# Performance work log

Hardware: AMD Instinct MI355X
Metric: run time of the kernel (lower is better)

## Reference

```python
import jax, jax.numpy as jnp
import numpy as np

B, L, D, H = 4, 2048, 512, 8
DH = D // H

def cdist(x):
    # torch.cdist(x, x) with p=2: (b,l,l) euclidean distances over feature dim
    sq = jnp.sum(x * x, axis=-1)  # (b,l)
    d2 = sq[:, :, None] + sq[:, None, :] - 2.0 * jnp.einsum('bld,bmd->blm', x, x)
    return jnp.sqrt(jnp.maximum(d2, 0.0))

def distance_residual_bias(cd, mask2d):
    # raw_max=True branch
    Dm = cd * mask2d
    row_max = jnp.max(Dm, axis=-1, keepdims=True)  # (b,l,1)
    Dm = row_max - Dm
    eye = jnp.eye(Dm.shape[-1], dtype=Dm.dtype)
    Dm = Dm * (1.0 - eye)  # zero diagonal
    return Dm * mask2d

def layernorm(x, g, b, eps=1e-5):
    mu = jnp.mean(x, axis=-1, keepdims=True)
    var = jnp.mean((x - mu) ** 2, axis=-1, keepdims=True)
    return (x - mu) * jax.lax.rsqrt(var + eps) * g + b

def setup_inputs() -> dict:
    key = jax.random.key(0)
    ks = jax.random.split(key, 16)
    s = lambda k, shape: jax.random.normal(k, shape, dtype=jnp.float32) * 0.02
    inp = {
        'x': jax.random.normal(ks[0], (B, L, D), dtype=jnp.float32),
        'node_mask': jnp.ones((B, L), dtype=jnp.float32),
        'wq': s(ks[1], (D, D)), 'bq': jnp.zeros((D,), jnp.float32),
        'wk': s(ks[2], (D, D)), 'bk': jnp.zeros((D,), jnp.float32),
        'wv': s(ks[3], (D, D)), 'bv': jnp.zeros((D,), jnp.float32),
        'wo': s(ks[4], (D, D)), 'bo': jnp.zeros((D,), jnp.float32),
        'ln1_g': jnp.ones((D,), jnp.float32), 'ln1_b': jnp.zeros((D,), jnp.float32),
        'w1': s(ks[5], (D, 4 * D)), 'b1': jnp.zeros((4 * D,), jnp.float32),
        'w2': s(ks[6], (4 * D, D)), 'b2': jnp.zeros((D,), jnp.float32),
        'ln2_g': jnp.ones((D,), jnp.float32), 'ln2_b': jnp.zeros((D,), jnp.float32),
    }
    return inp

def reference(x, node_mask, wq, bq, wk, bk, wv, bv, wo, bo,
              ln1_g, ln1_b, w1, b1, w2, b2, ln2_g, ln2_b):
    b, l, d = x.shape
    mask2d = node_mask[:, :, None] * node_mask[:, None, :]  # (b,l,l)
    bias = distance_residual_bias(cdist(x), mask2d)          # (b,l,l)

    q = (x @ wq + bq).reshape(b, l, H, DH).transpose(0, 2, 1, 3)
    k = (x @ wk + bk).reshape(b, l, H, DH).transpose(0, 2, 1, 3)
    v = (x @ wv + bv).reshape(b, l, H, DH).transpose(0, 2, 1, 3)
    scores = jnp.einsum('bhqd,bhkd->bhqk', q, k) / jnp.sqrt(jnp.float32(DH))
    scores = scores + bias[:, None, :, :]  # broadcast distance bias over heads
    attn = jax.nn.softmax(scores, axis=-1)
    y = jnp.einsum('bhqk,bhkd->bhqd', attn, v).transpose(0, 2, 1, 3).reshape(b, l, d)
    y = y @ wo + bo

    X = layernorm(x + y, ln1_g, ln1_b)            # AddNorm 1 (dropout=eval/no-op)
    ffn = jax.nn.relu(X @ w1 + b1) @ w2 + b2      # PositionWiseFFN
    X = layernorm(X + ffn, ln2_g, ln2_b)          # AddNorm 2
    return X
```

## Files before the change

### kernel.cpp

```cpp
#include <hip/hip_runtime.h>
#include <stdint.h>

#define GAS __attribute__((address_space(1)))
#define LAS __attribute__((address_space(3)))

typedef __attribute__((ext_vector_type(8))) __bf16 bf16x8;
typedef __attribute__((ext_vector_type(4))) float f32x4;

static constexpr int Bb = 4, Ll = 2048, Dd = 512, Hh = 8, DHd = 64;
static constexpr float LOG2E = 1.4426950408889634f;

__device__ __forceinline__ unsigned short f2bf(float f){
  unsigned u = __float_as_uint(f);
  u += 0x7fffu + ((u >> 16) & 1u);
  return (unsigned short)(u >> 16);
}
__device__ __forceinline__ void gload16(const void* g, void* l){
  __builtin_amdgcn_global_load_lds((const GAS void*)g, (LAS void*)l, 16, 0, 0);
}
__device__ __forceinline__ f32x4 mfma16(bf16x8 a, bf16x8 b, f32x4 c){
  return __builtin_amdgcn_mfma_f32_16x16x32_bf16(a, b, c, 0, 0, 0);
}
__device__ __forceinline__ float exp2_hw(float x){
  float r; asm("v_exp_f32 %0, %1" : "=v"(r) : "v"(x)); return r;
}

__global__ __launch_bounds__(256) void sumsq_cast(const float* __restrict__ x,
                                                  unsigned short* __restrict__ xbf,
                                                  float* __restrict__ sq){
  int row = blockIdx.x, tid = threadIdx.x;
  float2 v = ((const float2*)(x + (size_t)row * Dd))[tid];
  ((unsigned*)(xbf + (size_t)row * Dd))[tid] =
      (unsigned)f2bf(v.x) | ((unsigned)f2bf(v.y) << 16);
  float s2 = v.x * v.x + v.y * v.y;
  #pragma unroll
  for (int t = 1; t < 64; t <<= 1) s2 += __shfl_xor(s2, t, 64);
  __shared__ float red[4];
  if ((tid & 63) == 0) red[tid >> 6] = s2;
  __syncthreads();
  if (tid == 0) sq[row] = red[0] + red[1] + red[2] + red[3];
}

__global__ void transpose_all(
    const float* __restrict__ wq, const float* __restrict__ wk,
    const float* __restrict__ wv, const float* __restrict__ wo,
    const float* __restrict__ w1, const float* __restrict__ w2,
    unsigned short* __restrict__ wqkvT, unsigned short* __restrict__ woT,
    unsigned short* __restrict__ w1T, unsigned short* __restrict__ w2T)
{
  __shared__ float t[32][33];
  int bid = blockIdx.x;
  const float* in; unsigned short* out; int R, C, bx, by;
  if (bid < 1024){
    int s = bid >> 8, tt = bid & 255;
    in  = s == 0 ? wq : s == 1 ? wk : s == 2 ? wv : wo;
    out = s == 3 ? woT : wqkvT + s * 512 * 512;
    R = 512; C = 512; bx = tt & 15; by = tt >> 4;
  } else if (bid < 2048){
    int tt = bid - 1024; in = w1; out = w1T; R = 512; C = 2048; bx = tt & 63; by = tt >> 6;
  } else {
    int tt = bid - 2048; in = w2; out = w2T; R = 2048; C = 512; bx = tt & 15; by = tt >> 4;
  }
  int tx = threadIdx.x, ty = threadIdx.y;
  int c0 = bx * 32, r0 = by * 32;
  #pragma unroll
  for (int j = 0; j < 32; j += 8) t[ty + j][tx] = in[(size_t)(r0 + ty + j) * C + c0 + tx];
  __syncthreads();
  #pragma unroll
  for (int j = 0; j < 32; j += 8) out[(size_t)(c0 + ty + j) * R + r0 + tx] = f2bf(t[tx][ty + j]);
}

__global__ __launch_bounds__(256) void v_transpose(const unsigned short* __restrict__ qkv,
                                                   unsigned short* __restrict__ vT){
  int b = blockIdx.z, h = blockIdx.y, l0 = blockIdx.x * 64;
  int tid = threadIdx.x;
  __shared__ unsigned short t[64 * 64];
  #pragma unroll
  for (int it = 0; it < 2; ++it){
    int row = tid >> 2;
    int c = (tid & 3) + it * 4;
    uint4 d = *(const uint4*)(qkv + (size_t)(b * Ll + l0 + row) * 1536 + 1024 + h * DHd + c * 8);
    *(uint4*)((char*)t + row * 128 + ((c ^ (row & 7)) << 4)) = d;
  }
  __syncthreads();
  #pragma unroll
  for (int it = 0; it < 2; ++it){
    int dh = tid >> 2;
    int c2 = (tid & 3) + it * 4;
    unsigned pk[4];
    #pragma unroll
    for (int p = 0; p < 4; ++p){
      unsigned short e0, e1;
      {
        int ll = c2 * 8 + p * 2;
        e0 = *(const unsigned short*)((const char*)t + ll * 128 +
              ((((dh >> 3) ^ (ll & 7))) << 4) + ((dh & 7) << 1));
        ll = c2 * 8 + p * 2 + 1;
        e1 = *(const unsigned short*)((const char*)t + ll * 128 +
              ((((dh >> 3) ^ (ll & 7))) << 4) + ((dh & 7) << 1));
      }
      pk[p] = (unsigned)e0 | ((unsigned)e1 << 16);
    }
    uint4 o; o.x = pk[0]; o.y = pk[1]; o.z = pk[2]; o.w = pk[3];
    *(uint4*)(vT + ((size_t)(b * Hh + h) * DHd + dh) * Ll + l0 + c2 * 8) = o;
  }
}

template<int MODE>
__global__ __launch_bounds__(256) void gemm_bt(
    const unsigned short* __restrict__ A,
    const unsigned short* __restrict__ Bt,
    int M, int N, int K,
    const float* __restrict__ bias,
    const float* __restrict__ extra,
    float* __restrict__ outf,
    unsigned short* __restrict__ outb,
    const float* __restrict__ sq,
    float* __restrict__ rmax,
    const float* __restrict__ mask,
    const float* __restrict__ bias_k,
    const float* __restrict__ bias_v)
{
  int m0, n0, bxx = 0, byy = 0;
  if (MODE == 0){
    int z = blockIdx.z;
    A    += (size_t)z * Ll * Dd;
    Bt    = A;
    outb += (size_t)z * Ll * Ll;
    sq += z * Ll; rmax += z * Ll; mask += z * Ll;
    int tt = blockIdx.x, byv = 0;
    while (tt >= 16 - byv){ tt -= 16 - byv; byv++; }
    byy = byv; bxx = byv + tt;
    m0 = byy * 128; n0 = bxx * 128;
  } else {
    m0 = blockIdx.y * 128; n0 = blockIdx.x * 128;
  }
  if (MODE == 6){
    int z = blockIdx.z;
    A    += (size_t)z * (K >> 1);
    Bt   += (size_t)z * (K >> 1);
    outf += (size_t)z * (size_t)M * N;
  }
  const int KL = (MODE == 6) ? (K >> 1) : K;
  const int tid = threadIdx.x, w = tid >> 6, l = tid & 63;
  const int wm = w >> 1, wn = w & 1;
  __shared__ unsigned short lA[2][128 * 64];
  __shared__ unsigned short lB[2][128 * 64];
  f32x4 acc[4][4];
  const f32x4 z4 = {0.f, 0.f, 0.f, 0.f};
  #pragma unroll
  for (int i = 0; i < 4; i++){
    #pragma unroll
    for (int j = 0; j < 4; j++) acc[i][j] = z4;
  }
  const int srow = w * 8 + (l >> 3);
  const int sc = l & 7;

  #pragma unroll
  for (int j = 0; j < 4; j++){
    int row = j * 32 + srow;
    gload16(A + (size_t)(m0 + row) * K + ((sc ^ (row & 7)) << 3),
            &lA[0][0] + j * 2048 + w * 512);
    gload16(Bt + (size_t)(n0 + row) * K + ((sc ^ (row & 7)) << 3),
            &lB[0][0] + j * 2048 + w * 512);
  }
  __syncthreads();

  int cur = 0;
  for (int k0 = 0; k0 < KL; k0 += 64, cur ^= 1){
    if (k0 + 64 < KL){
      #pragma unroll
      for (int j = 0; j < 4; j++){
        int row = j * 32 + srow;
        gload16(A + (size_t)(m0 + row) * K + k0 + 64 + ((sc ^ (row & 7)) << 3),
                &lA[cur ^ 1][0] + j * 2048 + w * 512);
        gload16(Bt + (size_t)(n0 + row) * K + k0 + 64 + ((sc ^ (row & 7)) << 3),
                &lB[cur ^ 1][0] + j * 2048 + w * 512);
      }
    }
    bf16x8 af[4][2], bv[4][2];
    #pragma unroll
    for (int kk = 0; kk < 2; kk++){
      #pragma unroll
      for (int f = 0; f < 4; f++){
        int ra = wm * 64 + f * 16 + (l & 15);
        af[f][kk] = *(const bf16x8*)((const char*)&lA[cur][0] + ra * 128 +
                      (((kk * 4 + (l >> 4)) ^ (ra & 7)) << 4));
        int rb = wn * 64 + f * 16 + (l & 15);
        bv[f][kk] = *(const bf16x8*)((const char*)&lB[cur][0] + rb * 128 +
                      (((kk * 4 + (l >> 4)) ^ (rb & 7)) << 4));
      }
    }
    #pragma unroll
    for (int mf = 0; mf < 4; mf++){
      #pragma unroll
      for (int nf = 0; nf < 4; nf++){
        #pragma unroll
        for (int kk = 0; kk < 2; kk++)
          acc[mf][nf] = mfma16(af[mf][kk], bv[nf][kk], acc[mf][nf]);
      }
    }
    __syncthreads();
  }

  if (MODE == 0){
    float sqc[4], mkc[4];
    #pragma unroll
    for (int nf = 0; nf < 4; nf++){
      int col = n0 + wn * 64 + nf * 16 + (l & 15);
      sqc[nf] = sq[col]; mkc[nf] = mask[col];
    }
    #pragma unroll
    for (int mf = 0; mf < 4; mf++){
      #pragma unroll
      for (int r = 0; r < 4; r++){
        int row = m0 + wm * 64 + mf * 16 + (l >> 4) * 4 + r;
        float sqi = sq[row], mi = mask[row];
        #pragma unroll
        for (int nf = 0; nf < 4; nf++){
          float d2 = sqi + sqc[nf] - 2.f * acc[mf][nf][r];
          acc[mf][nf][r] = sqrtf(fmaxf(d2, 0.f)) * (mi * mkc[nf]) * LOG2E + 8.f;
        }
      }
    }
    #pragma unroll
    for (int mf = 0; mf < 4; mf++){
      #pragma unroll
      for (int r = 0; r < 4; r++){
        int row = m0 + wm * 64 + mf * 16 + (l >> 4) * 4 + r;
        float rm = 0.f;
        #pragma unroll
        for (int nf = 0; nf < 4; nf++){
          int col = n0 + wn * 64 + nf * 16 + (l & 15);
          outb[(size_t)row * Ll + col] = f2bf(acc[mf][nf][r]);
          rm = fmaxf(rm, acc[mf][nf][r]);
        }
        #pragma unroll
        for (int t = 1; t < 16; t <<= 1) rm = fmaxf(rm, __shfl_xor(rm, t, 64));
        if ((l & 15) == 0) atomicMax((int*)(rmax + row), __float_as_int(rm));
      }
    }
    if (bxx != byy){
      #pragma unroll
      for (int nf = 0; nf < 4; nf++){
        int col = n0 + wn * 64 + nf * 16 + (l & 15);
        float cm = 0.f;
        #pragma unroll
        for (int mf = 0; mf < 4; mf++){
          uint2 pk2;
          pk2.x = (unsigned)f2bf(acc[mf][nf][0]) | ((unsigned)f2bf(acc[mf][nf][1]) << 16);
          pk2.y = (unsigned)f2bf(acc[mf][nf][2]) | ((unsigned)f2bf(acc[mf][nf][3]) << 16);
          int rowb = m0 + wm * 64 + mf * 16 + (l >> 4) * 4;
          *(uint2*)(outb + (size_t)col * Ll + rowb) = pk2;
          cm = fmaxf(cm, fmaxf(fmaxf(acc[mf][nf][0], acc[mf][nf][1]),
                               fmaxf(acc[mf][nf][2], acc[mf][nf][3])));
        }
        cm = fmaxf(cm, __shfl_xor(cm, 16, 64));
        cm = fmaxf(cm, __shfl_xor(cm, 32, 64));
        if ((l >> 4) == 0) atomicMax((int*)(rmax + col), __float_as_int(cm));
      }
    }
  } else {
    #pragma unroll
    for (int mf = 0; mf < 4; mf++){
      #pragma unroll
      for (int r = 0; r < 4; r++){
        int row = m0 + wm * 64 + mf * 16 + (l >> 4) * 4 + r;
        #pragma unroll
        for (int nf = 0; nf < 4; nf++){
          int col = n0 + wn * 64 + nf * 16 + (l & 15);
          if (MODE == 6){
            outf[(size_t)row * N + col] = acc[mf][nf][r];
          } else {
            float bval;
            if (MODE == 5){
              const float* bp = col < 512 ? bias : (col < 1024 ? bias_k : bias_v);
              bval = bp[col & 511];
            } else {
              bval = bias[col];
            }
            float v = acc[mf][nf][r] + bval;
            if (MODE == 3) outb[(size_t)row * N + col] = f2bf(fmaxf(v, 0.f));
            if (MODE == 5) outb[(size_t)row * N + col] = f2bf(v);
            if (MODE == 2)
              outf[(size_t)row * N + col] = v + extra[(size_t)row * N + col];
          }
        }
      }
    }
  }
}

__global__ __launch_bounds__(256, 4) void flash_attn(
    const unsigned short* __restrict__ qkv,
    const unsigned short* __restrict__ vT,
    const unsigned short* __restrict__ cdm,
    const float* __restrict__ rmax,
    unsigned short* __restrict__ y)
{
  const int b = blockIdx.z, h = blockIdx.y, q0 = blockIdx.x * 64;
  const int tid = threadIdx.x, w = tid >> 6, l = tid & 63;
  const int ql = l & 15, lg = l >> 4;
  __shared__ unsigned short QPs[64 * 64];
  __shared__ unsigned short Ks[2][64 * 64];
  __shared__ unsigned short Vs[2][64 * 64];

  const int srow = w * 8 + (l >> 3);
  const int sc = l & 7;
  const unsigned short* kbase = qkv + (size_t)b * Ll * 1536 + 512 + h * DHd;
  const unsigned short* vbase = vT + (size_t)(b * Hh + h) * DHd * Ll;

  #pragma unroll
  for (int j = 0; j < 2; j++){
    int row = j * 32 + srow;
    gload16(qkv + (size_t)(b * Ll + q0 + row) * 1536 + h * DHd + ((sc ^ (row & 7)) << 3),
            QPs + j * 2048 + w * 512);
    gload16(kbase + (size_t)row * 1536 + ((sc ^ (row & 7)) << 3),
            &Ks[0][0] + j * 2048 + w * 512);
    gload16(vbase + (size_t)row * Ll + ((sc ^ (row & 7)) << 3),
            &Vs[0][0] + j * 2048 + w * 512);
  }

  const int qg = q0 + w * 16 + ql;
  const float rmx8 = rmax[b * Ll + qg] - 8.f;
  const unsigned short* cdrow = cdm + (size_t)(b * Ll + qg) * Ll;

  uint2 cdn[4];
  #pragma unroll
  for (int nf = 0; nf < 4; nf++)
    cdn[nf] = *(const uint2*)(cdrow + nf * 16 + lg * 4);

  f32x4 o[4];
  const f32x4 z4 = {0.f, 0.f, 0.f, 0.f};
  #pragma unroll
  for (int nf = 0; nf < 4; nf++) o[nf] = z4;
  float lsum = 0.f;

  __syncthreads();

  bf16x8 qa[2];
  #pragma unroll
  for (int kk = 0; kk < 2; kk++){
    int ra = w * 16 + ql;
    qa[kk] = *(const bf16x8*)((const char*)QPs + ra * 128 +
               (((kk * 4 + lg) ^ (ql & 7)) << 4));
  }

  const int NT = Ll / 64;
  for (int t = 0; t < NT; ++t){
    const int k0 = t * 64;
    const int cur = t & 1;

    uint2 cdc[4];
    #pragma unroll
    for (int nf = 0; nf < 4; nf++) cdc[nf] = cdn[nf];

    if (t + 1 < NT){
      const int kn = k0 + 64;
      #pragma unroll
      for (int nf = 0; nf < 4; nf++)
        cdn[nf] = *(const uint2*)(cdrow + kn + nf * 16 + lg * 4);
      #pragma unroll
      for (int j = 0; j < 2; j++){
        int row = j * 32 + srow;
        gload16(kbase + (size_t)(kn + row) * 1536 + ((sc ^ (row & 7)) << 3),
                &Ks[cur ^ 1][0] + j * 2048 + w * 512);
        gload16(vbase + (size_t)row * Ll + kn + ((sc ^ (row & 7)) << 3),
                &Vs[cur ^ 1][0] + j * 2048 + w * 512);
      }
    }

    f32x4 s[4];
    #pragma unroll
    for (int nf = 0; nf < 4; nf++){
      s[nf] = z4;
      #pragma unroll
      for (int kk = 0; kk < 2; kk++){
        int rb = nf * 16 + ql;
        bf16x8 kb = *(const bf16x8*)((const char*)Ks[cur] + rb * 128 +
                      (((kk * 4 + lg) ^ (ql & 7)) << 4));
        s[nf] = mfma16(kb, qa[kk], s[nf]);
      }
    }

    float sv[16];
    #pragma unroll
    for (int nf = 0; nf < 4; nf++){
      float c0 = __uint_as_float(cdc[nf].x << 16);
      float c1 = __uint_as_float(cdc[nf].x & 0xffff0000u);
      float c2 = __uint_as_float(cdc[nf].y << 16);
      float c3 = __uint_as_float(cdc[nf].y & 0xffff0000u);
      sv[nf * 4 + 0] = fmaf(s[nf][0], 0.125f * LOG2E, -c0);
      sv[nf * 4 + 1] = fmaf(s[nf][1], 0.125f * LOG2E, -c1);
      sv[nf * 4 + 2] = fmaf(s[nf][2], 0.125f * LOG2E, -c2);
      sv[nf * 4 + 3] = fmaf(s[nf][3], 0.125f * LOG2E, -c3);
    }
    if (k0 == q0){
      #pragma unroll
      for (int nf = 0; nf < 4; nf++) if (nf == w){
        #pragma unroll
        for (int r = 0; r < 4; r++)
          if (lg * 4 + r == ql) sv[nf * 4 + r] -= rmx8;
      }
    }

    float p[16], ps = 0.f;
    #pragma unroll
    for (int i = 0; i < 16; i++){ p[i] = exp2_hw(sv[i]); ps += p[i]; }
    lsum += ps;

    #pragma unroll
    for (int nf = 0; nf < 4; nf++){
      unsigned d0, d1;
      asm("v_cvt_pk_bf16_f32 %0, %1, %2" : "=v"(d0) : "v"(p[nf*4+0]), "v"(p[nf*4+1]));
      asm("v_cvt_pk_bf16_f32 %0, %1, %2" : "=v"(d1) : "v"(p[nf*4+2]), "v"(p[nf*4+3]));
      uint2 pk2; pk2.x = d0; pk2.y = d1;
      *(uint2*)((char*)QPs + w * 2048 + ql * 128 +
                ((nf * 32 + lg * 8) ^ ((ql & 7) << 4))) = pk2;
    }

    bf16x8 pa[2];
    #pragma unroll
    for (int kk = 0; kk < 2; kk++)
      pa[kk] = *(const bf16x8*)((const char*)QPs + w * 2048 + ql * 128 +
                 ((((kk * 4 + lg)) ^ (ql & 7)) << 4));
    #pragma unroll
    for (int nf = 0; nf < 4; nf++){
      #pragma unroll
      for (int kk = 0; kk < 2; kk++){
        int rv = nf * 16 + ql;
        bf16x8 vb = *(const bf16x8*)((const char*)Vs[cur] + rv * 128 +
                      (((kk * 4 + lg) ^ (ql & 7)) << 4));
        o[nf] = mfma16(pa[kk], vb, o[nf]);
      }
    }
    __syncthreads();
  }

  float ltot = lsum;
  ltot += __shfl_xor(ltot, 16, 64);
  ltot += __shfl_xor(ltot, 32, 64);
  float lf[4];
  #pragma unroll
  for (int r = 0; r < 4; r++)
    lf[r] = __shfl(ltot, (l & 48) | (lg * 4 + r), 64);
  #pragma unroll
  for (int nf = 0; nf < 4; nf++){
    #pragma unroll
    for (int r = 0; r < 4; r++){
      int qo = q0 + w * 16 + lg * 4 + r;
      float v = o[nf][r] / lf[r];
      y[(size_t)(b * Ll + qo) * Dd + h * DHd + nf * 16 + ql] = f2bf(v);
    }
  }
}

__global__ __launch_bounds__(256) void ln_kernel(const float* __restrict__ in,
                                                 const float* __restrict__ g,
                                                 const float* __restrict__ bt,
                                                 float* __restrict__ outf,
                                                 unsigned short* __restrict__ outb){
  int row = blockIdx.x, tid = threadIdx.x;
  float2 v = ((const float2*)(in + (size_t)row * Dd))[tid];
  float s = v.x + v.y, s2 = v.x * v.x + v.y * v.y;
  #pragma unroll
  for (int t = 1; t < 64; t <<= 1){ s += __shfl_xor(s, t, 64); s2 += __shfl_xor(s2, t, 64); }
  __shared__ float red[8];
  if ((tid & 63) == 0){ red[tid >> 6] = s; red[4 + (tid >> 6)] = s2; }
  __syncthreads();
  float S  = red[0] + red[1] + red[2] + red[3];
  float S2 = red[4] + red[5] + red[6] + red[7];
  float mu = S * (1.f / 512.f);
  float var = fmaxf(S2 * (1.f / 512.f) - mu * mu, 0.f);
  float rs = rsqrtf(var + 1e-5f);
  int c = tid * 2;
  float o0 = (v.x - mu) * rs * g[c] + bt[c];
  float o1 = (v.y - mu) * rs * g[c + 1] + bt[c + 1];
  float2 ov; ov.x = o0; ov.y = o1;
  ((float2*)(outf + (size_t)row * Dd))[tid] = ov;
  if (outb){
    ((unsigned*)(outb + (size_t)row * Dd))[tid] =
        (unsigned)f2bf(o0) | ((unsigned)f2bf(o1) << 16);
  }
}

__global__ __launch_bounds__(256) void ln2p_kernel(
    const float* __restrict__ p01,
    const float* __restrict__ bias,
    const float* __restrict__ extra,
    const float* __restrict__ g, const float* __restrict__ bt,
    float* __restrict__ outf)
{
  int row = blockIdx.x, tid = threadIdx.x;
  float2 a0 = ((const float2*)(p01 + (size_t)row * Dd))[tid];
  float2 a1 = ((const float2*)(p01 + (size_t)Bb * Ll * Dd + (size_t)row * Dd))[tid];
  float2 ex = ((const float2*)(extra + (size_t)row * Dd))[tid];
  int c = tid * 2;
  float vx = a0.x + a1.x + bias[c]     + ex.x;
  float vy = a0.y + a1.y + bias[c + 1] + ex.y;
  float s = vx + vy, s2 = vx * vx + vy * vy;
  #pragma unroll
  for (int t = 1; t < 64; t <<= 1){ s += __shfl_xor(s, t, 64); s2 += __shfl_xor(s2, t, 64); }
  __shared__ float red[8];
  if ((tid & 63) == 0){ red[tid >> 6] = s; red[4 + (tid >> 6)] = s2; }
  __syncthreads();
  float S  = red[0] + red[1] + red[2] + red[3];
  float S2 = red[4] + red[5] + red[6] + red[7];
  float mu = S * (1.f / 512.f);
  float var = fmaxf(S2 * (1.f / 512.f) - mu * mu, 0.f);
  float rs = rsqrtf(var + 1e-5f);
  float o0 = (vx - mu) * rs * g[c] + bt[c];
  float o1 = (vy - mu) * rs * g[c + 1] + bt[c + 1];
  float2 ov; ov.x = o0; ov.y = o1;
  ((float2*)(outf + (size_t)row * Dd))[tid] = ov;
}

extern "C" void kernel_launch(void* const* d_in, const int* in_sizes, int n_in,
                              void* d_out, int out_size, void* d_ws, size_t ws_size,
                              hipStream_t stream){
  const float* x     = (const float*)d_in[0];
  const float* nmask = (const float*)d_in[1];
  const float* wq = (const float*)d_in[2];  const float* bq = (const float*)d_in[3];
  const float* wk = (const float*)d_in[4];  const float* bk = (const float*)d_in[5];
  const float* wv = (const float*)d_in[6];  const float* bv = (const float*)d_in[7];
  const float* wo = (const float*)d_in[8];  const float* bo = (const float*)d_in[9];
  const float* ln1g = (const float*)d_in[10]; const float* ln1b = (const float*)d_in[11];
  const float* w1 = (const float*)d_in[12]; const float* b1 = (const float*)d_in[13];
  const float* w2 = (const float*)d_in[14]; const float* b2 = (const float*)d_in[15];
  const float* ln2g = (const float*)d_in[16]; const float* ln2b = (const float*)d_in[17];
  float* outp = (float*)d_out;
  char* ws = (char*)d_ws;

  unsigned short* xbf   = (unsigned short*)(ws + 0);
  float* sq   = (float*)(ws + 8388608);
  float* rmax = (float*)(ws + 8421376);
  unsigned short* wqkvT = (unsigned short*)(ws + 8454144);
  unsigned short* woT   = (unsigned short*)(ws + 10027008);
  unsigned short* w1T   = (unsigned short*)(ws + 10551296);
  unsigned short* w2T   = (unsigned short*)(ws + 12648448);
  unsigned short* cdm   = (unsigned short*)(ws + 14745600);
  unsigned short* qkv   = (unsigned short*)(ws + 48300032);
  unsigned short* vT    = (unsigned short*)(ws + 73465856);
  unsigned short* yb    = (unsigned short*)(ws + 81854464);
  float* res = (float*)(ws + 90243072);
  float* Xf  = (float*)(ws + 107020288);
  unsigned short* h1  = cdm;
  unsigned short* Xbf = qkv;
  float* p01 = (float*)qkv;

  hipMemsetAsync(rmax, 0, sizeof(float) * Bb * Ll, stream);

  sumsq_cast<<<Bb * Ll, 256, 0, stream>>>(x, xbf, sq);

  transpose_all<<<3072, dim3(32, 8), 0, stream>>>(wq, wk, wv, wo, w1, w2,
                                                  wqkvT, woT, w1T, w2T);

  gemm_bt<0><<<dim3(136, 1, 4), 256, 0, stream>>>(xbf, xbf, Ll, Ll, Dd,
      nullptr, nullptr, nullptr, cdm, sq, rmax, nmask, nullptr, nullptr);

  gemm_bt<5><<<dim3(12, 64, 1), 256, 0, stream>>>(xbf, wqkvT, Bb * Ll, 1536, Dd,
      bq, nullptr, nullptr, qkv, nullptr, nullptr, nullptr, bk, bv);

  v_transpose<<<dim3(Ll / 64, Hh, Bb), 256, 0, stream>>>(qkv, vT);

  flash_attn<<<dim3(Ll / 64, Hh, Bb), 256, 0, stream>>>(qkv, vT, cdm, rmax, yb);

  gemm_bt<2><<<dim3(4, 64, 1), 256, 0, stream>>>(yb, woT, Bb * Ll, Dd, Dd,
      bo, x, res, nullptr, nullptr, nullptr, nullptr, nullptr, nullptr);

  ln_kernel<<<Bb * Ll, 256, 0, stream>>>(res, ln1g, ln1b, Xf, Xbf);

  gemm_bt<3><<<dim3(16, 64, 1), 256, 0, stream>>>(Xbf, w1T, Bb * Ll, 4 * Dd, Dd,
      b1, nullptr, nullptr, h1, nullptr, nullptr, nullptr, nullptr, nullptr);
  gemm_bt<6><<<dim3(4, 64, 2), 256, 0, stream>>>(h1, w2T, Bb * Ll, Dd, 4 * Dd,
      nullptr, nullptr, p01, nullptr, nullptr, nullptr, nullptr, nullptr, nullptr);

  ln2p_kernel<<<Bb * Ll, 256, 0, stream>>>(p01, b2, Xf, ln2g, ln2b, outp);
}
```

Measured before the change: 251.5 us.

## Merge prep kernels, add MFMA priority hints, drop fp32 LN1 output

```diff
diff --git a/kernel.cpp b/kernel.cpp
--- a/kernel.cpp
+++ b/kernel.cpp
@@ -25,31 +25,31 @@
   float r; asm("v_exp_f32 %0, %1" : "=v"(r) : "v"(x)); return r;
 }
 
-__global__ __launch_bounds__(256) void sumsq_cast(const float* __restrict__ x,
-                                                  unsigned short* __restrict__ xbf,
-                                                  float* __restrict__ sq){
-  int row = blockIdx.x, tid = threadIdx.x;
-  float2 v = ((const float2*)(x + (size_t)row * Dd))[tid];
-  ((unsigned*)(xbf + (size_t)row * Dd))[tid] =
-      (unsigned)f2bf(v.x) | ((unsigned)f2bf(v.y) << 16);
-  float s2 = v.x * v.x + v.y * v.y;
-  #pragma unroll
-  for (int t = 1; t < 64; t <<= 1) s2 += __shfl_xor(s2, t, 64);
-  __shared__ float red[4];
-  if ((tid & 63) == 0) red[tid >> 6] = s2;
-  __syncthreads();
-  if (tid == 0) sq[row] = red[0] + red[1] + red[2] + red[3];
-}
-
-__global__ void transpose_all(
+__global__ __launch_bounds__(256) void prep_all(
+    const float* __restrict__ x,
     const float* __restrict__ wq, const float* __restrict__ wk,
     const float* __restrict__ wv, const float* __restrict__ wo,
     const float* __restrict__ w1, const float* __restrict__ w2,
+    unsigned short* __restrict__ xbf, float* __restrict__ sq,
     unsigned short* __restrict__ wqkvT, unsigned short* __restrict__ woT,
     unsigned short* __restrict__ w1T, unsigned short* __restrict__ w2T)
 {
   __shared__ float t[32][33];
+  __shared__ float red[4];
   int bid = blockIdx.x;
+  if (bid >= 3072){
+    int row = bid - 3072, tid = threadIdx.x;
+    float2 v = ((const float2*)(x + (size_t)row * Dd))[tid];
+    ((unsigned*)(xbf + (size_t)row * Dd))[tid] =
+        (unsigned)f2bf(v.x) | ((unsigned)f2bf(v.y) << 16);
+    float s2 = v.x * v.x + v.y * v.y;
+    #pragma unroll
+    for (int s = 1; s < 64; s <<= 1) s2 += __shfl_xor(s2, s, 64);
+    if ((tid & 63) == 0) red[tid >> 6] = s2;
+    __syncthreads();
+    if (tid == 0) sq[row] = red[0] + red[1] + red[2] + red[3];
+    return;
+  }
   const float* in; unsigned short* out; int R, C, bx, by;
   if (bid < 1024){
     int s = bid >> 8, tt = bid & 255;
@@ -61,7 +61,7 @@
   } else {
     int tt = bid - 2048; in = w2; out = w2T; R = 2048; C = 512; bx = tt & 15; by = tt >> 4;
   }
-  int tx = threadIdx.x, ty = threadIdx.y;
+  int tx = threadIdx.x & 31, ty = threadIdx.x >> 5;
   int c0 = bx * 32, r0 = by * 32;
   #pragma unroll
   for (int j = 0; j < 32; j += 8) t[ty + j][tx] = in[(size_t)(r0 + ty + j) * C + c0 + tx];
@@ -371,6 +371,7 @@
     }
 
     f32x4 s[4];
+    __builtin_amdgcn_s_setprio(1);
     #pragma unroll
     for (int nf = 0; nf < 4; nf++){
       s[nf] = z4;
@@ -382,6 +383,7 @@
         s[nf] = mfma16(kb, qa[kk], s[nf]);
       }
     }
+    __builtin_amdgcn_s_setprio(0);
 
     float sv[16];
     #pragma unroll
@@ -424,6 +426,7 @@
     for (int kk = 0; kk < 2; kk++)
       pa[kk] = *(const bf16x8*)((const char*)QPs + w * 2048 + ql * 128 +
                  ((((kk * 4 + lg)) ^ (ql & 7)) << 4));
+    __builtin_amdgcn_s_setprio(1);
     #pragma unroll
     for (int nf = 0; nf < 4; nf++){
       #pragma unroll
@@ -434,6 +437,7 @@
         o[nf] = mfma16(pa[kk], vb, o[nf]);
       }
     }
+    __builtin_amdgcn_s_setprio(0);
     __syncthreads();
   }
 
@@ -458,7 +462,6 @@
 __global__ __launch_bounds__(256) void ln_kernel(const float* __restrict__ in,
                                                  const float* __restrict__ g,
                                                  const float* __restrict__ bt,
-                                                 float* __restrict__ outf,
                                                  unsigned short* __restrict__ outb){
   int row = blockIdx.x, tid = threadIdx.x;
   float2 v = ((const float2*)(in + (size_t)row * Dd))[tid];
@@ -476,28 +479,26 @@
   int c = tid * 2;
   float o0 = (v.x - mu) * rs * g[c] + bt[c];
   float o1 = (v.y - mu) * rs * g[c + 1] + bt[c + 1];
-  float2 ov; ov.x = o0; ov.y = o1;
-  ((float2*)(outf + (size_t)row * Dd))[tid] = ov;
-  if (outb){
-    ((unsigned*)(outb + (size_t)row * Dd))[tid] =
-        (unsigned)f2bf(o0) | ((unsigned)f2bf(o1) << 16);
-  }
+  ((unsigned*)(outb + (size_t)row * Dd))[tid] =
+      (unsigned)f2bf(o0) | ((unsigned)f2bf(o1) << 16);
 }
 
 __global__ __launch_bounds__(256) void ln2p_kernel(
     const float* __restrict__ p01,
     const float* __restrict__ bias,
-    const float* __restrict__ extra,
+    const unsigned short* __restrict__ extra,
     const float* __restrict__ g, const float* __restrict__ bt,
     float* __restrict__ outf)
 {
   int row = blockIdx.x, tid = threadIdx.x;
   float2 a0 = ((const float2*)(p01 + (size_t)row * Dd))[tid];
   float2 a1 = ((const float2*)(p01 + (size_t)Bb * Ll * Dd + (size_t)row * Dd))[tid];
-  float2 ex = ((const float2*)(extra + (size_t)row * Dd))[tid];
+  unsigned ex = ((const unsigned*)(extra + (size_t)row * Dd))[tid];
+  float ex0 = __uint_as_float(ex << 16);
+  float ex1 = __uint_as_float(ex & 0xffff0000u);
   int c = tid * 2;
-  float vx = a0.x + a1.x + bias[c]     + ex.x;
-  float vy = a0.y + a1.y + bias[c + 1] + ex.y;
+  float vx = a0.x + a1.x + bias[c]     + ex0;
+  float vy = a0.y + a1.y + bias[c + 1] + ex1;
   float s = vx + vy, s2 = vx * vx + vy * vy;
   #pragma unroll
   for (int t = 1; t < 64; t <<= 1){ s += __shfl_xor(s, t, 64); s2 += __shfl_xor(s2, t, 64); }
@@ -543,17 +544,14 @@
   unsigned short* vT    = (unsigned short*)(ws + 73465856);
   unsigned short* yb    = (unsigned short*)(ws + 81854464);
   float* res = (float*)(ws + 90243072);
-  float* Xf  = (float*)(ws + 107020288);
+  float* p01 = res;
   unsigned short* h1  = cdm;
   unsigned short* Xbf = qkv;
-  float* p01 = (float*)qkv;
 
   hipMemsetAsync(rmax, 0, sizeof(float) * Bb * Ll, stream);
 
-  sumsq_cast<<<Bb * Ll, 256, 0, stream>>>(x, xbf, sq);
-
-  transpose_all<<<3072, dim3(32, 8), 0, stream>>>(wq, wk, wv, wo, w1, w2,
-                                                  wqkvT, woT, w1T, w2T);
+  prep_all<<<3072 + Bb * Ll, 256, 0, stream>>>(x, wq, wk, wv, wo, w1, w2,
+                                               xbf, sq, wqkvT, woT, w1T, w2T);
 
   gemm_bt<0><<<dim3(136, 1, 4), 256, 0, stream>>>(xbf, xbf, Ll, Ll, Dd,
       nullptr, nullptr, nullptr, cdm, sq, rmax, nmask, nullptr, nullptr);
@@ -568,12 +566,12 @@
   gemm_bt<2><<<dim3(4, 64, 1), 256, 0, stream>>>(yb, woT, Bb * Ll, Dd, Dd,
       bo, x, res, nullptr, nullptr, nullptr, nullptr, nullptr, nullptr);
 
-  ln_kernel<<<Bb * Ll, 256, 0, stream>>>(res, ln1g, ln1b, Xf, Xbf);
+  ln_kernel<<<Bb * Ll, 256, 0, stream>>>(res, ln1g, ln1b, Xbf);
 
   gemm_bt<3><<<dim3(16, 64, 1), 256, 0, stream>>>(Xbf, w1T, Bb * Ll, 4 * Dd, Dd,
       b1, nullptr, nullptr, h1, nullptr, nullptr, nullptr, nullptr, nullptr);
   gemm_bt<6><<<dim3(4, 64, 2), 256, 0, stream>>>(h1, w2T, Bb * Ll, Dd, 4 * Dd,
       nullptr, nullptr, p01, nullptr, nullptr, nullptr, nullptr, nullptr, nullptr);
 
-  ln2p_kernel<<<Bb * Ll, 256, 0, stream>>>(p01, b2, Xf, ln2g, ln2b, outp);
-}
+  ln2p_kernel<<<Bb * Ll, 256, 0, stream>>>(p01, b2, Xbf, ln2g, ln2b, outp);
+}
```

Result: no change. 252.8 us (+0.5%).
